# Performance work log

Measured on AMD Instinct MI355X. Metric: run time of the kernel, lower is better.

## Reference

```python
import jax, jax.numpy as jnp
import numpy as np

ALPHA = 0.2  # LeakyReLU negative slope
NEG_INF = -9e15


def setup_inputs() -> dict:
    key = jax.random.key(0)
    k1, k2, k3, k4, k5 = jax.random.split(key, 5)
    B, N, F_in, F_out = 1, 8192, 256, 128
    h = jax.random.normal(k1, (B, N, F_in), dtype=jnp.float32)
    adj_mat = jax.random.randint(k2, (B, N, N), 0, 2, dtype=jnp.int32)
    W = jax.random.normal(k3, (F_out, F_in), dtype=jnp.float32) * 0.05
    b = jax.random.normal(k4, (F_out,), dtype=jnp.float32) * 0.05
    a = jax.random.normal(k5, (2 * F_out, 1), dtype=jnp.float32) * 0.05
    return {"h": h, "adj_mat": adj_mat, "W": W, "b": b, "a": a}


def reference(h, adj_mat, W, b, a):
    # Wh: (B, N, F_out)
    Wh = jnp.einsum('bnf,of->bno', h, W) + b
    F_out = W.shape[0]
    # Original builds concat[Wh_i, Wh_j] @ a. Equivalent: a1.Wh_i + a2.Wh_j.
    a1 = a[:F_out, 0]
    a2 = a[F_out:, 0]
    s1 = Wh @ a1  # (B, N) source-i contribution
    s2 = Wh @ a2  # (B, N) source-j contribution
    e = s1[:, :, None] + s2[:, None, :]  # (B, N, N)
    e = jnp.where(e >= 0, e, ALPHA * e)  # LeakyReLU
    e = jnp.where(adj_mat > 0, e, NEG_INF)
    attention = jax.nn.softmax(e, axis=1)  # softmax over dim=1, as in the source
    h_prime = jnp.einsum('bij,bjf->bif', attention, Wh)
    return jax.nn.elu(h_prime)
```

## Files before the change

kernel.cpp:

```cpp
#include <hip/hip_runtime.h>

#define NN 8192
#define FI 256
#define FO 128
#define GAT_ALPHA 0.2f

typedef _Float16 f16x8 __attribute__((ext_vector_type(8)));
typedef _Float16 f16x2 __attribute__((ext_vector_type(2)));
typedef float f32x4 __attribute__((ext_vector_type(4)));
typedef unsigned char uchar;
typedef unsigned int uint32;

__global__ __launch_bounds__(256) void k1s_scores(const float* __restrict__ h,
                                                  const float* __restrict__ W,
                                                  const float* __restrict__ bias,
                                                  const float* __restrict__ a,
                                                  float4* __restrict__ r4,
                                                  float4* __restrict__ c4,
                                                  float2* __restrict__ r2,
                                                  _Float16* __restrict__ ey16,
                                                  _Float16* __restrict__ ez16,
                                                  float* __restrict__ s2x,
                                                  float* __restrict__ corr) {
  __shared__ __align__(16) float wa1[FI];
  __shared__ __align__(16) float wa2[FI];
  __shared__ float cb[2];
  const int t = threadIdx.x;
  const int j0 = blockIdx.x * 32;
  if (blockIdx.x == 0 && t < FO) corr[t] = 0.f;
  {
    float sa = 0.f, sb = 0.f;
    for (int f = 0; f < FO; ++f) {
      const float w = W[(size_t)f * FI + t];
      sa += a[f] * w;
      sb += a[FO + f] * w;
    }
    wa1[t] = sa;
    wa2[t] = sb;
  }
  if (t < 64) {
    float c1 = bias[t] * a[t] + bias[t + 64] * a[t + 64];
    float c2 = bias[t] * a[FO + t] + bias[t + 64] * a[FO + t + 64];
#pragma unroll
    for (int o = 32; o >= 1; o >>= 1) {
      c1 += __shfl_xor(c1, o);
      c2 += __shfl_xor(c2, o);
    }
    if (t == 0) { cb[0] = c1; cb[1] = c2; }
  }
  __syncthreads();
  const int lane = t & 63, wv = t >> 6;
  const float4 w1v = *(const float4*)&wa1[lane * 4];
  const float4 w2v = *(const float4*)&wa2[lane * 4];
  const float cb1 = cb[0], cb2 = cb[1];
#pragma unroll
  for (int rr = 0; rr < 8; ++rr) {
    const int j = j0 + wv * 8 + rr;
    const float4 hv = *(const float4*)&h[(size_t)j * FI + lane * 4];
    float s1 = hv.x * w1v.x + hv.y * w1v.y + hv.z * w1v.z + hv.w * w1v.w;
    float s2 = hv.x * w2v.x + hv.y * w2v.y + hv.z * w2v.z + hv.w * w2v.w;
#pragma unroll
    for (int o = 32; o >= 1; o >>= 1) {
      s1 += __shfl_xor(s1, o);
      s2 += __shfl_xor(s2, o);
    }
    if (lane == 0) {
      s1 += cb1;
      s2 += cb2;
      const float e1 = expf(s1), e1a = expf(GAT_ALPHA * s1);
      const float e2 = expf(s2), e2a = expf(GAT_ALPHA * s2);
      float4 rv; rv.x = s1; rv.y = e1; rv.z = e1a; rv.w = 0.f;
      float4 cv; cv.x = s2; cv.y = e2; cv.z = e2a; cv.w = 0.f;
      r4[j] = rv;
      c4[j] = cv;
      r2[j] = make_float2(e1, e1a);
      ey16[j] = (_Float16)e2;
      ez16[j] = (_Float16)e2a;
      s2x[j] = s2;
    }
  }
}

__global__ __launch_bounds__(256) void mega(const int* __restrict__ adj,
                                            const float* __restrict__ h,
                                            const float* __restrict__ W,
                                            const float* __restrict__ bias,
                                            const float4* __restrict__ r4,
                                            const float* __restrict__ s2x,
                                            uchar* __restrict__ bitsB,
                                            float2* __restrict__ zpart,
                                            float* __restrict__ Wh) {
  __shared__ __align__(16) char smem[33536];
  const int t = threadIdx.x;
  if (blockIdx.x < 512) {
    float4* rs = (float4*)smem;
    const int jc = blockIdx.x & 3;
    const int ic = blockIdx.x >> 2;
    const int i0 = ic * 64;
    const int j0 = jc * 2048 + t * 8;
    if (t < 64) rs[t] = r4[i0 + t];
    const float4 ca = *(const float4*)(s2x + j0);
    const float4 cbv = *(const float4*)(s2x + j0 + 4);
    const float cx[8] = {ca.x, ca.y, ca.z, ca.w, cbv.x, cbv.y, cbv.z, cbv.w};
    float accP[8], accN[8];
#pragma unroll
    for (int e = 0; e < 8; ++e) { accP[e] = 0.f; accN[e] = 0.f; }
    __syncthreads();
    const int4* ap = (const int4*)(adj + (size_t)i0 * NN + j0);
    uchar* bp = bitsB + (size_t)i0 * (NN / 8) + jc * 256 + t;
    for (int ir = 0; ir < 64; ir += 8) {
      int4 av[8][2];
#pragma unroll
      for (int u = 0; u < 8; ++u) {
        av[u][0] = ap[(size_t)(ir + u) * (NN / 4)];
        av[u][1] = ap[(size_t)(ir + u) * (NN / 4) + 1];
      }
#pragma unroll
      for (int u = 0; u < 8; ++u) {
        const float4 ri = rs[ir + u];
        const int aa[8] = {av[u][0].x, av[u][0].y, av[u][0].z, av[u][0].w,
                           av[u][1].x, av[u][1].y, av[u][1].z, av[u][1].w};
        uint32 byte = 0;
#pragma unroll
        for (int e = 0; e < 8; ++e) {
          const bool act = aa[e] > 0;
          byte |= act ? (1u << e) : 0u;
          const bool pos = (ri.x + cx[e]) >= 0.f;
          accP[e] += (act && pos) ? ri.y : 0.f;
          accN[e] += (act && !pos) ? ri.z : 0.f;
        }
        bp[(size_t)(ir + u) * (NN / 8)] = (uchar)byte;
      }
    }
    float2* zp = zpart + (size_t)ic * NN + j0;
#pragma unroll
    for (int e = 0; e < 8; ++e) zp[e] = make_float2(accP[e], accN[e]);
  } else {
    typedef float4 hs4row_t[65];
    typedef float wtrow_t[132];
    hs4row_t* hs4 = (hs4row_t*)smem;
    wtrow_t* wt = (wtrow_t*)(smem + 16640);
    const int bid = blockIdx.x - 512;
    const int j0 = bid * 16;
#pragma unroll
    for (int e = 0; e < 4; ++e) {
      const int i = t + 256 * e;
      const int row = i >> 6, q = i & 63;
      hs4[row][q] = *(const float4*)(h + (size_t)(j0 + row) * FI + 4 * q);
    }
    const int f4 = (t & 31) * 4;
    const int r0 = (t >> 5) * 2;
    float acc[2][4];
#pragma unroll
    for (int r = 0; r < 2; ++r)
#pragma unroll
      for (int e = 0; e < 4; ++e) acc[r][e] = 0.f;

    for (int kc = 0; kc < FI; kc += 32) {
      __syncthreads();
      {
        const int f = t >> 1, kb = (t & 1) * 16;
        const float* wsrc = W + (size_t)f * FI + kc + kb;
#pragma unroll
        for (int e = 0; e < 4; ++e) {
          const float4 wv = *(const float4*)(wsrc + 4 * e);
          wt[kb + 4 * e + 0][f] = wv.x;
          wt[kb + 4 * e + 1][f] = wv.y;
          wt[kb + 4 * e + 2][f] = wv.z;
          wt[kb + 4 * e + 3][f] = wv.w;
        }
      }
      __syncthreads();
#pragma unroll
      for (int kk = 0; kk < 8; ++kk) {
        float4 wv[4];
#pragma unroll
        for (int i = 0; i < 4; ++i) wv[i] = *(const float4*)&wt[4 * kk + i][f4];
        float4 hv[2];
#pragma unroll
        for (int r = 0; r < 2; ++r) hv[r] = hs4[r0 + r][(kc >> 2) + kk];
#pragma unroll
        for (int r = 0; r < 2; ++r) {
          acc[r][0] += hv[r].x * wv[0].x + hv[r].y * wv[1].x + hv[r].z * wv[2].x + hv[r].w * wv[3].x;
          acc[r][1] += hv[r].x * wv[0].y + hv[r].y * wv[1].y + hv[r].z * wv[2].y + hv[r].w * wv[3].y;
          acc[r][2] += hv[r].x * wv[0].z + hv[r].y * wv[1].z + hv[r].z * wv[2].z + hv[r].w * wv[3].z;
          acc[r][3] += hv[r].x * wv[0].w + hv[r].y * wv[1].w + hv[r].z * wv[2].w + hv[r].w * wv[3].w;
        }
      }
    }
    const float4 bv = *(const float4*)&bias[f4];
#pragma unroll
    for (int r = 0; r < 2; ++r) {
      float4 o;
      o.x = acc[r][0] + bv.x;
      o.y = acc[r][1] + bv.y;
      o.z = acc[r][2] + bv.z;
      o.w = acc[r][3] + bv.w;
      *(float4*)&Wh[(size_t)(j0 + r0 + r) * FO + f4] = o;
    }
  }
}

__global__ __launch_bounds__(256) void k3_scale(const float* __restrict__ Wh,
                                                const float4* __restrict__ c4,
                                                const float2* __restrict__ zpart,
                                                _Float16* __restrict__ Wfrag,
                                                float* __restrict__ corr) {
  __shared__ float rz[64];
  __shared__ int emp[64];
  __shared__ float2 psum[256];
  __shared__ __align__(16) _Float16 tile[FO * 64];
  const int t = threadIdx.x;
  const int j0 = blockIdx.x * 64;
  {
    const int jl = t & 63, q = t >> 6;
    float p = 0.f, n = 0.f;
    for (int ic = q * 32; ic < q * 32 + 32; ++ic) {
      const float2 z = zpart[(size_t)ic * NN + j0 + jl];
      p += z.x;
      n += z.y;
    }
    psum[t] = make_float2(p, n);
  }
  __syncthreads();
  if (t < 64) {
    const float p = psum[t].x + psum[64 + t].x + psum[128 + t].x + psum[192 + t].x;
    const float n = psum[t].y + psum[64 + t].y + psum[128 + t].y + psum[192 + t].y;
    const float4 cj = c4[j0 + t];
    const float Z = cj.y * p + cj.z * n;
    rz[t] = (Z > 0.f) ? 1.f / Z : 0.f;
    emp[t] = (Z > 0.f) ? 0 : 1;
  }
  __syncthreads();
  const int f = t & 127, half = t >> 7;
  const unsigned swf = (unsigned)((f & 7) << 4);
  for (int r = half; r < 64; r += 2) {
    const float v = Wh[(size_t)(j0 + r) * FO + f];
    *(_Float16*)((char*)tile + f * 128 + (((unsigned)(r * 2)) ^ swf)) =
        (_Float16)(v * rz[r]);
    if (emp[r]) atomicAdd(&corr[f], v * (1.f / 8192.f));
  }
  __syncthreads();
#pragma unroll
  for (int q = 0; q < 4; ++q) {
    const int G = t + 256 * q;
    const int kcfb = G >> 6, gl = G & 63;
    const int kc = kcfb >> 3, fb = kcfb & 7;
    const int gf = fb * 16 + (gl & 15);
    const int jloc = kc * 32 + (gl >> 4) * 8;
    const f16x8 v = *(const f16x8*)((const char*)tile + gf * 128 +
                                    (((unsigned)(jloc * 2)) ^ ((unsigned)((gf & 7) << 4))));
    ((f16x8*)Wfrag)[(size_t)(((j0 >> 5) + kc) * 8 + fb) * 64 + gl] = v;
  }
}

#define BARRIER_LDS()                                          \
  do {                                                         \
    __builtin_amdgcn_sched_barrier(0);                         \
    asm volatile("s_waitcnt lgkmcnt(0)" ::: "memory");         \
    __builtin_amdgcn_s_barrier();                              \
    __builtin_amdgcn_sched_barrier(0);                         \
  } while (0)

__global__ __launch_bounds__(256) void k4_main(const uchar* __restrict__ bitsB,
                                               const float2* __restrict__ r2,
                                               const _Float16* __restrict__ ey16,
                                               const _Float16* __restrict__ ez16,
                                               const _Float16* __restrict__ Wfrag,
                                               float* __restrict__ part) {
  __shared__ __align__(16) _Float16 P[2][32 * 64];
  __shared__ uint32 lut[256][4];
  const int t = threadIdx.x;
  const int rowtile = blockIdx.x >> 2;
  const int kq = blockIdx.x & 3;
  const int rowbase = rowtile * 32;
  const int koff = kq * 2048;

  {
#pragma unroll
    for (int p = 0; p < 4; ++p) {
      const uint32 lo = ((t >> (2 * p)) & 1) ? 0x0000FFFFu : 0u;
      const uint32 hi = ((t >> (2 * p + 1)) & 1) ? 0xFFFF0000u : 0u;
      lut[t][p] = lo | hi;
    }
  }

  const int pr = t >> 3, jq = t & 7;
  const float2 rr = r2[rowbase + pr];
  const f16x2 rx2 = {(_Float16)rr.x, (_Float16)rr.x};
  const f16x2 ry2 = {(_Float16)rr.y, (_Float16)rr.y};
  const uchar* bp = bitsB + (size_t)(rowbase + pr) * (NN / 8) + (koff >> 3) + jq;
  const _Float16* eyp = ey16 + koff + jq * 8;
  const _Float16* ezp = ez16 + koff + jq * 8;
  char* const pdst0 = (char*)&P[0][0] + pr * 128 + (((unsigned)(jq * 16)) ^ ((unsigned)((pr & 7) << 4)));
  char* const pdst1 = (char*)&P[1][0] + pr * 128 + (((unsigned)(jq * 16)) ^ ((unsigned)((pr & 7) << 4)));

  const int lane = t & 63, wc = t >> 6;
  const int kgrp = lane >> 4, l15 = lane & 15;
  const unsigned asw = (unsigned)((l15 & 7) << 4);
  const int ar0 = l15 * 128;
  const int ar1 = ar0 + 16 * 128;

  f32x4 acc00 = {0.f, 0.f, 0.f, 0.f}, acc01 = {0.f, 0.f, 0.f, 0.f};
  f32x4 acc10 = {0.f, 0.f, 0.f, 0.f}, acc11 = {0.f, 0.f, 0.f, 0.f};

  uchar mb0, mb1;
  uint4 ey0, ez0, ey1, ez1;
  f16x8 B000, B001, B010, B011, B100, B101, B110, B111;

#define LOADALL(S, MB, EY, EZ, Bq00, Bq01, Bq10, Bq11)                              \
  do {                                                                              \
    MB = bp[(S) * 8];                                                               \
    EY = *(const uint4*)(eyp + (S) * 64);                                           \
    EZ = *(const uint4*)(ezp + (S) * 64);                                           \
    const _Float16* _b = Wfrag + ((size_t)((kq * 64 + (S) * 2) * 8 + wc * 2) * 64 + lane) * 8; \
    Bq00 = *(const f16x8*)(_b);                                                     \
    Bq01 = *(const f16x8*)(_b + 512);                                               \
    Bq10 = *(const f16x8*)(_b + 4096);                                              \
    Bq11 = *(const f16x8*)(_b + 4096 + 512);                                        \
  } while (0)

#define PGEN(DST, MB, EY, EZ)                                                        \
  do {                                                                               \
    const uint4 _m = *(const uint4*)(&lut[MB][0]);                                   \
    const uint32 _eys[4] = {EY.x, EY.y, EY.z, EY.w};                                 \
    const uint32 _ezs[4] = {EZ.x, EZ.y, EZ.z, EZ.w};                                 \
    const uint32 _ms[4] = {_m.x, _m.y, _m.z, _m.w};                                  \
    uint32 _o[4];                                                                    \
    _Pragma("unroll") for (int _p = 0; _p < 4; ++_p) {                               \
      const f16x2 _a = __builtin_bit_cast(f16x2, _eys[_p]) * rx2;                    \
      const f16x2 _b2 = __builtin_bit_cast(f16x2, _ezs[_p]) * ry2;                   \
      const f16x2 _mx = __builtin_elementwise_max(_a, _b2);                          \
      _o[_p] = __builtin_bit_cast(uint32, _mx) & _ms[_p];                            \
    }                                                                                \
    uint4 _st; _st.x = _o[0]; _st.y = _o[1]; _st.z = _o[2]; _st.w = _o[3];           \
    *(uint4*)(DST) = _st;                                                            \
  } while (0)

#define DO_MFMA(BUF, Bq00, Bq01, Bq10, Bq11)                                        \
  do {                                                                              \
    const char* _Pb = (const char*)&P[BUF][0];                                      \
    const f16x8 a00 = *(const f16x8*)(_Pb + ar0 + ((((unsigned)(kgrp * 16))) ^ asw));        \
    const f16x8 a01 = *(const f16x8*)(_Pb + ar0 + (((unsigned)(64 + kgrp * 16)) ^ asw));     \
    const f16x8 a10 = *(const f16x8*)(_Pb + ar1 + ((((unsigned)(kgrp * 16))) ^ asw));        \
    const f16x8 a11 = *(const f16x8*)(_Pb + ar1 + (((unsigned)(64 + kgrp * 16)) ^ asw));     \
    __builtin_amdgcn_s_setprio(1);                                                  \
    acc00 = __builtin_amdgcn_mfma_f32_16x16x32_f16(a00, Bq00, acc00, 0, 0, 0);      \
    acc01 = __builtin_amdgcn_mfma_f32_16x16x32_f16(a00, Bq01, acc01, 0, 0, 0);      \
    acc10 = __builtin_amdgcn_mfma_f32_16x16x32_f16(a10, Bq00, acc10, 0, 0, 0);      \
    acc11 = __builtin_amdgcn_mfma_f32_16x16x32_f16(a10, Bq01, acc11, 0, 0, 0);      \
    acc00 = __builtin_amdgcn_mfma_f32_16x16x32_f16(a01, Bq10, acc00, 0, 0, 0);      \
    acc01 = __builtin_amdgcn_mfma_f32_16x16x32_f16(a01, Bq11, acc01, 0, 0, 0);      \
    acc10 = __builtin_amdgcn_mfma_f32_16x16x32_f16(a11, Bq10, acc10, 0, 0, 0);      \
    acc11 = __builtin_amdgcn_mfma_f32_16x16x32_f16(a11, Bq11, acc11, 0, 0, 0);      \
    __builtin_amdgcn_s_setprio(0);                                                  \
  } while (0)

  LOADALL(0, mb0, ey0, ez0, B000, B001, B010, B011);
  LOADALL(1, mb1, ey1, ez1, B100, B101, B110, B111);
  __syncthreads();
  PGEN(pdst0, mb0, ey0, ez0);
  BARRIER_LDS();

  for (int s = 0; s < 32; s += 2) {
    PGEN(pdst1, mb1, ey1, ez1);
    DO_MFMA(0, B000, B001, B010, B011);
    if (s + 2 < 32) LOADALL(s + 2, mb0, ey0, ez0, B000, B001, B010, B011);
    BARRIER_LDS();
    DO_MFMA(1, B100, B101, B110, B111);
    if (s + 2 < 32) PGEN(pdst0, mb0, ey0, ez0);
    if (s + 3 < 32) LOADALL(s + 3, mb1, ey1, ez1, B100, B101, B110, B111);
    BARRIER_LDS();
  }

#undef LOADALL
#undef PGEN
#undef DO_MFMA

  const int orow = rowbase + kgrp * 4;
  const int ocol = wc * 32 + l15;
  float* aP = part + (size_t)kq * NN * FO + (size_t)orow * FO + ocol;
#pragma unroll
  for (int r = 0; r < 4; ++r) {
    aP[(size_t)r * FO] = acc00[r];
    aP[(size_t)r * FO + 16] = acc01[r];
    aP[(size_t)(16 + r) * FO] = acc10[r];
    aP[(size_t)(16 + r) * FO + 16] = acc11[r];
  }
}

__global__ __launch_bounds__(256) void k5_fin(const float* __restrict__ part,
                                              const float* __restrict__ corr,
                                              float* __restrict__ out) {
  const int idx = blockIdx.x * 256 + threadIdx.x;
  const float4 p0 = ((const float4*)part)[idx];
  const float4 p1 = ((const float4*)(part + (size_t)NN * FO))[idx];
  const float4 p2 = ((const float4*)(part + (size_t)2 * NN * FO))[idx];
  const float4 p3 = ((const float4*)(part + (size_t)3 * NN * FO))[idx];
  const float4 c = ((const float4*)corr)[idx & 31];
  float4 v;
  v.x = p0.x + p1.x + p2.x + p3.x + c.x;
  v.y = p0.y + p1.y + p2.y + p3.y + c.y;
  v.z = p0.z + p1.z + p2.z + p3.z + c.z;
  v.w = p0.w + p1.w + p2.w + p3.w + c.w;
  v.x = (v.x > 0.f) ? v.x : (expf(v.x) - 1.f);
  v.y = (v.y > 0.f) ? v.y : (expf(v.y) - 1.f);
  v.z = (v.z > 0.f) ? v.z : (expf(v.z) - 1.f);
  v.w = (v.w > 0.f) ? v.w : (expf(v.w) - 1.f);
  ((float4*)out)[idx] = v;
}

extern "C" void kernel_launch(void* const* d_in, const int* in_sizes, int n_in,
                              void* d_out, int out_size, void* d_ws, size_t ws_size,
                              hipStream_t stream) {
  const float* h = (const float*)d_in[0];
  const int* adj = (const int*)d_in[1];
  const float* W = (const float*)d_in[2];
  const float* b = (const float*)d_in[3];
  const float* a = (const float*)d_in[4];
  float* out = (float*)d_out;
  char* ws = (char*)d_ws;

  float* Wh = (float*)(ws + 0);
  _Float16* Wfrag = (_Float16*)(ws + 0x400000);
  uchar* bits = (uchar*)(ws + 0x600000);
  float2* zpart = (float2*)(ws + 0xE00000);
  float4* r4 = (float4*)(ws + 0x1600000);
  float4* c4 = (float4*)(ws + 0x1620000);
  float2* r2 = (float2*)(ws + 0x1640000);
  _Float16* ey16 = (_Float16*)(ws + 0x1650000);
  _Float16* ez16 = (_Float16*)(ws + 0x1654000);
  float* s2x = (float*)(ws + 0x1658000);
  float* corr = (float*)(ws + 0x1660000);
  float* part = (float*)(ws + 0x1700000);

  k1s_scores<<<NN / 32, 256, 0, stream>>>(h, W, b, a, r4, c4, r2, ey16, ez16, s2x, corr);
  mega<<<1024, 256, 0, stream>>>(adj, h, W, b, r4, s2x, bits, zpart, Wh);
  k3_scale<<<NN / 64, 256, 0, stream>>>(Wh, c4, zpart, Wfrag, corr);
  k4_main<<<1024, 256, 0, stream>>>(bits, r2, ey16, ez16, Wfrag, part);
  k5_fin<<<(NN * FO / 4) / 256, 256, 0, stream>>>(part, corr, out);
}
```

Before: 117.5 us.

## Generate attention A-fragments in registers, dropping LDS staging and barriers

The main kernel now has each wave build its MFMA A-operand fragments directly in registers from the ey/ez vectors and adjacency bitmask bytes, instead of writing the P tile to shared memory through a LUT and reading it back. This removes the shared-memory P buffers, the mask lookup table and every block barrier in the K loop. In exchange, each of the four waves redundantly recomputes the same 32x64 tile of probabilities (four times the VALU work for that step) and issues more small global loads for mask bytes and ey/ez values.

```diff
diff --git a/kernel.cpp b/kernel.cpp
--- a/kernel.cpp
+++ b/kernel.cpp
@@ -254,65 +254,48 @@
   }
 }
 
-#define BARRIER_LDS()                                          \
-  do {                                                         \
-    __builtin_amdgcn_sched_barrier(0);                         \
-    asm volatile("s_waitcnt lgkmcnt(0)" ::: "memory");         \
-    __builtin_amdgcn_s_barrier();                              \
-    __builtin_amdgcn_sched_barrier(0);                         \
-  } while (0)
-
 __global__ __launch_bounds__(256) void k4_main(const uchar* __restrict__ bitsB,
                                                const float2* __restrict__ r2,
                                                const _Float16* __restrict__ ey16,
                                                const _Float16* __restrict__ ez16,
                                                const _Float16* __restrict__ Wfrag,
                                                float* __restrict__ part) {
-  __shared__ __align__(16) _Float16 P[2][32 * 64];
-  __shared__ uint32 lut[256][4];
   const int t = threadIdx.x;
   const int rowtile = blockIdx.x >> 2;
   const int kq = blockIdx.x & 3;
   const int rowbase = rowtile * 32;
   const int koff = kq * 2048;
 
-  {
-#pragma unroll
-    for (int p = 0; p < 4; ++p) {
-      const uint32 lo = ((t >> (2 * p)) & 1) ? 0x0000FFFFu : 0u;
-      const uint32 hi = ((t >> (2 * p + 1)) & 1) ? 0xFFFF0000u : 0u;
-      lut[t][p] = lo | hi;
-    }
-  }
-
-  const int pr = t >> 3, jq = t & 7;
-  const float2 rr = r2[rowbase + pr];
-  const f16x2 rx2 = {(_Float16)rr.x, (_Float16)rr.x};
-  const f16x2 ry2 = {(_Float16)rr.y, (_Float16)rr.y};
-  const uchar* bp = bitsB + (size_t)(rowbase + pr) * (NN / 8) + (koff >> 3) + jq;
-  const _Float16* eyp = ey16 + koff + jq * 8;
-  const _Float16* ezp = ez16 + koff + jq * 8;
-  char* const pdst0 = (char*)&P[0][0] + pr * 128 + (((unsigned)(jq * 16)) ^ ((unsigned)((pr & 7) << 4)));
-  char* const pdst1 = (char*)&P[1][0] + pr * 128 + (((unsigned)(jq * 16)) ^ ((unsigned)((pr & 7) << 4)));
-
   const int lane = t & 63, wc = t >> 6;
   const int kgrp = lane >> 4, l15 = lane & 15;
-  const unsigned asw = (unsigned)((l15 & 7) << 4);
-  const int ar0 = l15 * 128;
-  const int ar1 = ar0 + 16 * 128;
+
+  const float2 rA = r2[rowbase + l15];
+  const float2 rB = r2[rowbase + 16 + l15];
+  const f16x2 rxA = {(_Float16)rA.x, (_Float16)rA.x};
+  const f16x2 ryA = {(_Float16)rA.y, (_Float16)rA.y};
+  const f16x2 rxB = {(_Float16)rB.x, (_Float16)rB.x};
+  const f16x2 ryB = {(_Float16)rB.y, (_Float16)rB.y};
+
+  const _Float16* eyp = ey16 + koff + kgrp * 8;
+  const _Float16* ezp = ez16 + koff + kgrp * 8;
+  const uchar* bpA = bitsB + (size_t)(rowbase + l15) * (NN / 8) + (koff >> 3) + kgrp;
+  const uchar* bpB = bitsB + (size_t)(rowbase + 16 + l15) * (NN / 8) + (koff >> 3) + kgrp;
 
   f32x4 acc00 = {0.f, 0.f, 0.f, 0.f}, acc01 = {0.f, 0.f, 0.f, 0.f};
   f32x4 acc10 = {0.f, 0.f, 0.f, 0.f}, acc11 = {0.f, 0.f, 0.f, 0.f};
 
-  uchar mb0, mb1;
-  uint4 ey0, ez0, ey1, ez1;
+  uint4 eyL0, eyH0, ezL0, ezH0, eyL1, eyH1, ezL1, ezH1;
+  uint32 bAL0, bAH0, bBL0, bBH0, bAL1, bAH1, bBL1, bBH1;
   f16x8 B000, B001, B010, B011, B100, B101, B110, B111;
 
-#define LOADALL(S, MB, EY, EZ, Bq00, Bq01, Bq10, Bq11)                              \
+#define LOADSTEP(S, EYL, EYH, EZL, EZH, BAL, BAH, BBL, BBH, Bq00, Bq01, Bq10, Bq11) \
   do {                                                                              \
-    MB = bp[(S) * 8];                                                               \
-    EY = *(const uint4*)(eyp + (S) * 64);                                           \
-    EZ = *(const uint4*)(ezp + (S) * 64);                                           \
+    EYL = *(const uint4*)(eyp + (S) * 64);                                          \
+    EYH = *(const uint4*)(eyp + (S) * 64 + 32);                                     \
+    EZL = *(const uint4*)(ezp + (S) * 64);                                          \
+    EZH = *(const uint4*)(ezp + (S) * 64 + 32);                                     \
+    BAL = bpA[(S) * 8]; BAH = bpA[(S) * 8 + 4];                                     \
+    BBL = bpB[(S) * 8]; BBH = bpB[(S) * 8 + 4];                                     \
     const _Float16* _b = Wfrag + ((size_t)((kq * 64 + (S) * 2) * 8 + wc * 2) * 64 + lane) * 8; \
     Bq00 = *(const f16x8*)(_b);                                                     \
     Bq01 = *(const f16x8*)(_b + 512);                                               \
@@ -320,30 +303,30 @@
     Bq11 = *(const f16x8*)(_b + 4096 + 512);                                        \
   } while (0)
 
-#define PGEN(DST, MB, EY, EZ)                                                        \
-  do {                                                                               \
-    const uint4 _m = *(const uint4*)(&lut[MB][0]);                                   \
-    const uint32 _eys[4] = {EY.x, EY.y, EY.z, EY.w};                                 \
-    const uint32 _ezs[4] = {EZ.x, EZ.y, EZ.z, EZ.w};                                 \
-    const uint32 _ms[4] = {_m.x, _m.y, _m.z, _m.w};                                  \
-    uint32 _o[4];                                                                    \
-    _Pragma("unroll") for (int _p = 0; _p < 4; ++_p) {                               \
-      const f16x2 _a = __builtin_bit_cast(f16x2, _eys[_p]) * rx2;                    \
-      const f16x2 _b2 = __builtin_bit_cast(f16x2, _ezs[_p]) * ry2;                   \
-      const f16x2 _mx = __builtin_elementwise_max(_a, _b2);                          \
-      _o[_p] = __builtin_bit_cast(uint32, _mx) & _ms[_p];                            \
-    }                                                                                \
-    uint4 _st; _st.x = _o[0]; _st.y = _o[1]; _st.z = _o[2]; _st.w = _o[3];           \
-    *(uint4*)(DST) = _st;                                                            \
+#define GENFRAG(OUT, BYT, EY, EZ, RX, RY)                                           \
+  do {                                                                              \
+    const uint32 _eys[4] = {EY.x, EY.y, EY.z, EY.w};                                \
+    const uint32 _ezs[4] = {EZ.x, EZ.y, EZ.z, EZ.w};                                \
+    union { uint32 u[4]; f16x8 v; } _U;                                             \
+    _Pragma("unroll") for (int _p = 0; _p < 4; ++_p) {                              \
+      const f16x2 _a = __builtin_bit_cast(f16x2, _eys[_p]) * RX;                    \
+      const f16x2 _b2 = __builtin_bit_cast(f16x2, _ezs[_p]) * RY;                   \
+      const f16x2 _mx = __builtin_elementwise_max(_a, _b2);                         \
+      const uint32 _lo = (uint32)((int)((BYT) << (31 - 2 * _p)) >> 31);             \
+      const uint32 _hi = (uint32)((int)((BYT) << (30 - 2 * _p)) >> 31);             \
+      const uint32 _m = (_lo & 0x0000FFFFu) | (_hi & 0xFFFF0000u);                  \
+      _U.u[_p] = __builtin_bit_cast(uint32, _mx) & _m;                              \
+    }                                                                               \
+    OUT = _U.v;                                                                     \
   } while (0)
 
-#define DO_MFMA(BUF, Bq00, Bq01, Bq10, Bq11)                                        \
+#define DOSTEP(EYL, EYH, EZL, EZH, BAL, BAH, BBL, BBH, Bq00, Bq01, Bq10, Bq11)      \
   do {                                                                              \
-    const char* _Pb = (const char*)&P[BUF][0];                                      \
-    const f16x8 a00 = *(const f16x8*)(_Pb + ar0 + ((((unsigned)(kgrp * 16))) ^ asw));        \
-    const f16x8 a01 = *(const f16x8*)(_Pb + ar0 + (((unsigned)(64 + kgrp * 16)) ^ asw));     \
-    const f16x8 a10 = *(const f16x8*)(_Pb + ar1 + ((((unsigned)(kgrp * 16))) ^ asw));        \
-    const f16x8 a11 = *(const f16x8*)(_Pb + ar1 + (((unsigned)(64 + kgrp * 16)) ^ asw));     \
+    f16x8 a00, a01, a10, a11;                                                       \
+    GENFRAG(a00, BAL, EYL, EZL, rxA, ryA);                                          \
+    GENFRAG(a01, BAH, EYH, EZH, rxA, ryA);                                          \
+    GENFRAG(a10, BBL, EYL, EZL, rxB, ryB);                                          \
+    GENFRAG(a11, BBH, EYH, EZH, rxB, ryB);                                          \
     __builtin_amdgcn_s_setprio(1);                                                  \
     acc00 = __builtin_amdgcn_mfma_f32_16x16x32_f16(a00, Bq00, acc00, 0, 0, 0);      \
     acc01 = __builtin_amdgcn_mfma_f32_16x16x32_f16(a00, Bq01, acc01, 0, 0, 0);      \
@@ -356,26 +339,21 @@
     __builtin_amdgcn_s_setprio(0);                                                  \
   } while (0)
 
-  LOADALL(0, mb0, ey0, ez0, B000, B001, B010, B011);
-  LOADALL(1, mb1, ey1, ez1, B100, B101, B110, B111);
-  __syncthreads();
-  PGEN(pdst0, mb0, ey0, ez0);
-  BARRIER_LDS();
+  LOADSTEP(0, eyL0, eyH0, ezL0, ezH0, bAL0, bAH0, bBL0, bBH0, B000, B001, B010, B011);
+  LOADSTEP(1, eyL1, eyH1, ezL1, ezH1, bAL1, bAH1, bBL1, bBH1, B100, B101, B110, B111);
 
   for (int s = 0; s < 32; s += 2) {
-    PGEN(pdst1, mb1, ey1, ez1);
-    DO_MFMA(0, B000, B001, B010, B011);
-    if (s + 2 < 32) LOADALL(s + 2, mb0, ey0, ez0, B000, B001, B010, B011);
-    BARRIER_LDS();
-    DO_MFMA(1, B100, B101, B110, B111);
-    if (s + 2 < 32) PGEN(pdst0, mb0, ey0, ez0);
-    if (s + 3 < 32) LOADALL(s + 3, mb1, ey1, ez1, B100, B101, B110, B111);
-    BARRIER_LDS();
-  }
-
-#undef LOADALL
-#undef PGEN
-#undef DO_MFMA
+    DOSTEP(eyL0, eyH0, ezL0, ezH0, bAL0, bAH0, bBL0, bBH0, B000, B001, B010, B011);
+    if (s + 2 < 32)
+      LOADSTEP(s + 2, eyL0, eyH0, ezL0, ezH0, bAL0, bAH0, bBL0, bBH0, B000, B001, B010, B011);
+    DOSTEP(eyL1, eyH1, ezL1, ezH1, bAL1, bAH1, bBL1, bBH1, B100, B101, B110, B111);
+    if (s + 3 < 32)
+      LOADSTEP(s + 3, eyL1, eyH1, ezL1, ezH1, bAL1, bAH1, bBL1, bBH1, B100, B101, B110, B111);
+  }
+
+#undef LOADSTEP
+#undef GENFRAG
+#undef DOSTEP
 
   const int orow = rowbase + kgrp * 4;
   const int ocol = wc * 32 + l15;
```

After: 174.4 us. 1.48x slower.
